# Kernel optimization log

Measured on AMD Instinct MI355X. Metric: run time of the kernel, lower is better.

## Reference

```python
import jax, jax.numpy as jnp
import numpy as np

D_MODEL = 1024
NUM_HEAD = 16
D_HEAD = 64
EPS = 1e-06


def setup_inputs() -> dict:
    key = jax.random.key(0)
    ks = jax.random.split(key, 16)
    d, h = D_MODEL, 4 * D_MODEL
    s = 1.0 / np.sqrt(d)
    inp = {
        "x": jax.random.normal(ks[0], (8, 1024, d), dtype=jnp.float32),
        # LayerNorm params
        "alpha1": jnp.ones((d,), jnp.float32),
        "beta1": jnp.zeros((d,), jnp.float32),
        "alpha2": jnp.ones((d,), jnp.float32),
        "beta2": jnp.zeros((d,), jnp.float32),
        # attention projections (weights stored as [in, out])
        "w_q": jax.random.normal(ks[1], (d, d), jnp.float32) * s,
        "b_q": jnp.zeros((d,), jnp.float32),
        "w_k": jax.random.normal(ks[2], (d, d), jnp.float32) * s,
        "b_k": jnp.zeros((d,), jnp.float32),
        "w_v": jax.random.normal(ks[3], (d, d), jnp.float32) * s,
        "b_v": jnp.zeros((d,), jnp.float32),
        "w_o": jax.random.normal(ks[4], (d, d), jnp.float32) * s,
        "b_o": jnp.zeros((d,), jnp.float32),
        # MLP
        "w1": jax.random.normal(ks[5], (d, h), jnp.float32) * s,
        "b1": jnp.zeros((h,), jnp.float32),
        "w2": jax.random.normal(ks[6], (h, d), jnp.float32) * (1.0 / np.sqrt(h)),
        "b2": jnp.zeros((d,), jnp.float32),
    }
    return inp


def _layer_norm(x, alpha, beta):
    mu = jnp.mean(x, axis=-1, keepdims=True)
    # torch .var() defaults to unbiased (ddof=1) — replicate exactly
    var = jnp.var(x, axis=-1, keepdims=True, ddof=1)
    return (x - mu) / jnp.sqrt(var + EPS) * alpha + beta


def _mha(x, w_q, b_q, w_k, b_k, w_v, b_v, w_o, b_o):
    b, p, _ = x.shape
    q = (x @ w_q + b_q).reshape(b, p, NUM_HEAD, D_HEAD).transpose(0, 2, 1, 3)
    k = (x @ w_k + b_k).reshape(b, p, NUM_HEAD, D_HEAD).transpose(0, 2, 1, 3)
    v = (x @ w_v + b_v).reshape(b, p, NUM_HEAD, D_HEAD).transpose(0, 2, 1, 3)
    scores = jnp.einsum("bhqd,bhkd->bhqk", q, k) / np.sqrt(D_HEAD).astype(np.float32)
    attn = jax.nn.softmax(scores, axis=-1)
    out = jnp.einsum("bhqk,bhkd->bhqd", attn, v)
    out = out.transpose(0, 2, 1, 3).reshape(b, p, NUM_HEAD * D_HEAD)
    return out @ w_o + b_o


def reference(x, alpha1, beta1, alpha2, beta2,
              w_q, b_q, w_k, b_k, w_v, b_v, w_o, b_o,
              w1, b1, w2, b2):
    # eval mode: Dropout is identity
    x = x + _mha(_layer_norm(x, alpha1, beta1), w_q, b_q, w_k, b_k, w_v, b_v, w_o, b_o)
    h = _layer_norm(x, alpha2, beta2)
    h = jax.nn.gelu(h @ w1 + b1, approximate=False)  # nn.GELU default: exact erf
    h = h @ w2 + b2
    return x + h
```

## Files before the change

kernel.cpp:

```cpp
#include <hip/hip_runtime.h>
#include <stdint.h>

typedef float f32x4 __attribute__((ext_vector_type(4)));
typedef short s16x8 __attribute__((ext_vector_type(8)));
typedef short s16x4 __attribute__((ext_vector_type(4)));
typedef unsigned int u32x4 __attribute__((ext_vector_type(4)));

#define M_TOTAL 8192
#define DM 1024
#define HID 4096
#define SEQ 1024
#define NH 16
#define DH 64

#define BAR() __builtin_amdgcn_s_barrier()
#define VMCNT8() do { asm volatile("s_waitcnt vmcnt(8)" ::: "memory"); __builtin_amdgcn_sched_barrier(0); } while (0)
#define VMCNT0() do { asm volatile("s_waitcnt vmcnt(0)" ::: "memory"); __builtin_amdgcn_sched_barrier(0); } while (0)
#define MFMA16 __builtin_amdgcn_mfma_f32_16x16x32_bf16

__device__ __forceinline__ unsigned short f2bf(float f) {
  unsigned int u = __float_as_uint(f);
  u = (u + 0x7fffu + ((u >> 16) & 1u)) >> 16;
  return (unsigned short)u;
}

__device__ __forceinline__ void gload16(const void* g, void* l) {
  __builtin_amdgcn_global_load_lds((__attribute__((address_space(1))) void*)g,
                                   (__attribute__((address_space(3))) void*)l,
                                   16, 0, 0);
}

__device__ __forceinline__ float erf_fast(float z) {
  const float az = fabsf(z);
  const float tt = 1.0f / fmaf(0.3275911f, az, 1.0f);
  float poly = fmaf(1.061405429f, tt, -1.453152027f);
  poly = fmaf(poly, tt, 1.421413741f);
  poly = fmaf(poly, tt, -0.284496736f);
  poly = fmaf(poly, tt, 0.254829592f);
  poly *= tt;
  const float e = __expf(-az * az);
  const float r = 1.0f - poly * e;
  return (z < 0.f) ? -r : r;
}

__global__ void tcast(const float* __restrict__ W, unsigned short* __restrict__ WT,
                      int K, int N) {
  __shared__ float tile[32][33];
  const int bn = blockIdx.x, bk = blockIdx.y;
  const int tx = threadIdx.x, ty = threadIdx.y;
#pragma unroll
  for (int i = 0; i < 32; i += 8)
    tile[ty + i][tx] = W[(size_t)(bk * 32 + ty + i) * N + bn * 32 + tx];
  __syncthreads();
#pragma unroll
  for (int i = 0; i < 32; i += 8)
    WT[(size_t)(bn * 32 + ty + i) * K + bk * 32 + tx] = f2bf(tile[tx][ty + i]);
}

__global__ __launch_bounds__(256)
void vtrans(const unsigned short* __restrict__ V, unsigned short* __restrict__ VT) {
  __shared__ unsigned short tile[64][65];
  const int bh = blockIdx.y, s0 = blockIdx.x * 64;
  const int t = threadIdx.x;
  const int sr = t >> 3, c0 = (t & 7) * 8;
#pragma unroll
  for (int it = 0; it < 2; ++it) {
    const int s = it * 32 + sr;
    const s16x8 v = *(const s16x8*)(V + ((size_t)bh * SEQ + s0 + s) * DH + c0);
#pragma unroll
    for (int i = 0; i < 8; ++i) tile[c0 + i][s] = (unsigned short)v[i];
  }
  __syncthreads();
#pragma unroll
  for (int it = 0; it < 2; ++it) {
    const int d = it * 32 + sr;
    s16x8 o;
#pragma unroll
    for (int i = 0; i < 8; ++i) o[i] = (short)tile[d][c0 + i];
    *(s16x8*)(VT + ((size_t)bh * DH + d) * SEQ + s0 + c0) = o;
  }
}

__global__ __launch_bounds__(256)
void ln_kernel(const float* __restrict__ x, const float* __restrict__ alpha,
               const float* __restrict__ beta, unsigned short* __restrict__ out) {
  const int row = blockIdx.x;
  const int t = threadIdx.x;
  const int w = t >> 6, lane = t & 63;
  const float4 v = ((const float4*)(x + (size_t)row * DM))[t];

  float s = v.x + v.y + v.z + v.w;
#pragma unroll
  for (int off = 32; off; off >>= 1) s += __shfl_xor(s, off, 64);
  __shared__ float red1[4];
  __shared__ float red2[4];
  if (lane == 0) red1[w] = s;
  __syncthreads();
  const float mu = (red1[0] + red1[1] + red1[2] + red1[3]) * (1.f / 1024.f);

  const float dx = v.x - mu, dy = v.y - mu, dz = v.z - mu, dw = v.w - mu;
  float sq = dx * dx + dy * dy + dz * dz + dw * dw;
#pragma unroll
  for (int off = 32; off; off >>= 1) sq += __shfl_xor(sq, off, 64);
  if (lane == 0) red2[w] = sq;
  __syncthreads();
  const float var = (red2[0] + red2[1] + red2[2] + red2[3]) * (1.f / 1023.f);
  const float rstd = rsqrtf(var + 1e-6f);

  const float4 a = ((const float4*)alpha)[t];
  const float4 b = ((const float4*)beta)[t];
  s16x4 o;
  o[0] = (short)f2bf(dx * rstd * a.x + b.x);
  o[1] = (short)f2bf(dy * rstd * a.y + b.y);
  o[2] = (short)f2bf(dz * rstd * a.z + b.z);
  o[3] = (short)f2bf(dw * rstd * a.w + b.w);
  *(s16x4*)(out + (size_t)row * DM + 4 * t) = o;
}

template <int MODE>
__device__ __forceinline__ void epi_store(int m, int n, float v, int Nout,
                                          unsigned short* __restrict__ obf, float* of,
                                          const float* res,
                                          const float* __restrict__ bias0,
                                          const float* __restrict__ bias1,
                                          const float* __restrict__ bias2) {
  if (MODE == 0) {
    const int which = n >> 10, nn = n & 1023;
    const float* bp = (which == 0) ? bias0 : ((which == 1) ? bias1 : bias2);
    v += bp[nn];
    const int b = m >> 10, s = m & 1023, h = nn >> 6, d = nn & 63;
    obf[(size_t)which * (M_TOTAL * DM) +
        (((size_t)(b * NH + h) * SEQ + s) * DH + d)] = f2bf(v);
  } else if (MODE == 1) {
    v += bias0[n] + res[(size_t)m * Nout + n];
    of[(size_t)m * Nout + n] = v;
  } else {
    v += bias0[n];
    const float gv = 0.5f * v * (1.0f + erf_fast(v * 0.70710678118654752f));
    obf[(size_t)m * Nout + n] = f2bf(gv);
  }
}

template <int MODE>
__global__ __launch_bounds__(256, 2)
void gemmk(const unsigned short* __restrict__ A, const unsigned short* __restrict__ B,
           int K, int Nout,
           unsigned short* __restrict__ obf, float* of, const float* res,
           const float* __restrict__ bias0, const float* __restrict__ bias1,
           const float* __restrict__ bias2) {
  __shared__ __attribute__((aligned(16))) unsigned short sA[2][128 * 64];
  __shared__ __attribute__((aligned(16))) unsigned short sB[2][128 * 64];
  const int t = threadIdx.x;
  const int lane = t & 63, wid = t >> 6;
  const int g = lane >> 4, r = lane & 15;
  const int wm = wid >> 1, wn = wid & 1;

  {
  }
  const int L = blockIdx.y * gridDim.x + blockIdx.x;
  const int nwg = gridDim.x * gridDim.y;
  const int chunk = nwg >> 3;
  const int ncols = chunk >> 6;
  const int denom = ncols << 3;
  const int xcd = L & 7, i = L >> 3;
  const int s = i / denom, w = i % denom;
  const int by = s * 8 + (w & 7);
  const int bx = xcd * ncols + (w >> 3);
  const int m0 = by * 128, n0 = bx * 128;

  const unsigned short* Ab = A + (size_t)m0 * K;
  const unsigned short* Bb = B + (size_t)n0 * K;

  const int rb = r & 7;
  const int slot0 = (g ^ rb) * 16;
  const int slot1 = ((4 + g) ^ rb) * 16;

  f32x4 acc[4][4];
#pragma unroll
  for (int i2 = 0; i2 < 4; ++i2)
#pragma unroll
    for (int j = 0; j < 4; ++j) acc[i2][j] = (f32x4){0.f, 0.f, 0.f, 0.f};

  auto stage = [&](int buf, int kt) {
#pragma unroll
    for (int s2 = 0; s2 < 4; ++s2) {
      const int f = s2 * 256 + t;
      const int row = f >> 3, c = f & 7;
      const int u = c ^ (row & 7);
      gload16(Ab + (size_t)row * K + kt * 64 + u * 8, &sA[buf][(size_t)row * 64 + c * 8]);
      gload16(Bb + (size_t)row * K + kt * 64 + u * 8, &sB[buf][(size_t)row * 64 + c * 8]);
    }
  };

  const int NT = K >> 6;
  stage(0, 0);
  stage(1, (NT > 1) ? 1 : 0);
  VMCNT8();
  BAR();

  for (int tt = 0; tt < NT; ++tt) {
    const int cur = tt & 1;
    const char* sAc = (const char*)&sA[cur][0];
    const char* sBc = (const char*)&sB[cur][0];

    s16x8 av[4][2], bv[4][2];
#pragma unroll
    for (int i2 = 0; i2 < 4; ++i2) {
      const int rbyte = (wm * 64 + i2 * 16 + r) * 128;
      av[i2][0] = *(const s16x8*)(sAc + rbyte + slot0);
      av[i2][1] = *(const s16x8*)(sAc + rbyte + slot1);
    }
#pragma unroll
    for (int n = 0; n < 4; ++n) {
      const int rbyte = (wn * 64 + n * 16 + r) * 128;
      bv[n][0] = *(const s16x8*)(sBc + rbyte + slot0);
      bv[n][1] = *(const s16x8*)(sBc + rbyte + slot1);
    }
#pragma unroll
    for (int i2 = 0; i2 < 4; ++i2)
#pragma unroll
      for (int n = 0; n < 4; ++n) {
        acc[i2][n] = MFMA16(av[i2][0], bv[n][0], acc[i2][n], 0, 0, 0);
        acc[i2][n] = MFMA16(av[i2][1], bv[n][1], acc[i2][n], 0, 0, 0);
      }

    BAR();
    const int tp2 = (tt + 2 < NT) ? tt + 2 : NT - 1;
    stage(cur, tp2);
    VMCNT8();
    BAR();
  }

  VMCNT0();

#pragma unroll
  for (int i2 = 0; i2 < 4; ++i2)
#pragma unroll
    for (int j = 0; j < 4; ++j) {
      const int m = m0 + wm * 64 + i2 * 16 + 4 * g + j;
#pragma unroll
      for (int nf = 0; nf < 4; ++nf) {
        const int n = n0 + wn * 64 + nf * 16 + r;
        epi_store<MODE>(m, n, acc[i2][nf][j], Nout, obf, of, res, bias0, bias1, bias2);
      }
    }
}

__global__ __launch_bounds__(256)
void attn_kernel(const unsigned short* __restrict__ QKV,
                 const unsigned short* __restrict__ VT,
                 unsigned short* __restrict__ O) {
  const unsigned short* Qg = QKV;
  const unsigned short* Kg = QKV + (size_t)M_TOTAL * DM;
  const int bh = blockIdx.y;
  const int q0 = blockIdx.x * 64;
  const int t = threadIdx.x, w = t >> 6, lane = t & 63;
  const int g = lane >> 4, r = lane & 15;
  const unsigned short* Qb = Qg + (size_t)bh * SEQ * DH;
  const unsigned short* Kb = Kg + (size_t)bh * SEQ * DH;
  const unsigned short* VTb = VT + (size_t)bh * DH * SEQ;

  __shared__ __attribute__((aligned(16))) unsigned short sK[2][64 * 64];
  __shared__ __attribute__((aligned(16))) unsigned short sV[2][64 * 64];

  s16x8 qf[2];
  {
    const unsigned short* qrow = Qb + (size_t)(q0 + w * 16 + r) * DH;
    qf[0] = *(const s16x8*)(qrow + g * 8);
    qf[1] = *(const s16x8*)(qrow + 32 + g * 8);
  }

  f32x4 oacc[4];
#pragma unroll
  for (int i = 0; i < 4; ++i) oacc[i] = (f32x4){0.f, 0.f, 0.f, 0.f};
  float mrun = -1e30f, lrun = 0.f;

  auto stage = [&](int buf, int kt) {
#pragma unroll
    for (int s2 = 0; s2 < 2; ++s2) {
      const int f = s2 * 256 + t;
      const int row = f >> 3, u = (f & 7) ^ (row & 7);
      gload16(Kb + (size_t)(kt * 64 + row) * DH + u * 8, &sK[buf][f * 8]);
      gload16(VTb + (size_t)row * SEQ + kt * 64 + u * 8, &sV[buf][f * 8]);
    }
  };

  stage(0, 0);
  __syncthreads();

  for (int kt = 0; kt < SEQ / 64; ++kt) {
    const int cur = kt & 1;
    if (kt < SEQ / 64 - 1) stage(cur ^ 1, kt + 1);

    f32x4 sc[4];
#pragma unroll
    for (int nf = 0; nf < 4; ++nf) {
      sc[nf] = (f32x4){0.f, 0.f, 0.f, 0.f};
      const int rowk = nf * 16 + r;
#pragma unroll
      for (int ks = 0; ks < 2; ++ks) {
        const int u = (4 * ks + g) ^ (rowk & 7);
        const s16x8 kf = *(const s16x8*)&sK[cur][rowk * 64 + u * 8];
        sc[nf] = __builtin_amdgcn_mfma_f32_16x16x32_bf16(kf, qf[ks], sc[nf], 0, 0, 0);
      }
    }

    float pm = -1e30f;
#pragma unroll
    for (int nf = 0; nf < 4; ++nf)
#pragma unroll
      for (int j = 0; j < 4; ++j) {
        sc[nf][j] *= 0.125f;
        pm = fmaxf(pm, sc[nf][j]);
      }
    pm = fmaxf(pm, __shfl_xor(pm, 16, 64));
    pm = fmaxf(pm, __shfl_xor(pm, 32, 64));

    const float mnew = fmaxf(mrun, pm);
    const float alpha = __expf(mrun - mnew);
    mrun = mnew;

    float p[4][4];
    float ps = 0.f;
#pragma unroll
    for (int nf = 0; nf < 4; ++nf)
#pragma unroll
      for (int j = 0; j < 4; ++j) {
        p[nf][j] = __expf(sc[nf][j] - mnew);
        ps += p[nf][j];
      }
    ps += __shfl_xor(ps, 16, 64);
    ps += __shfl_xor(ps, 32, 64);
    lrun = lrun * alpha + ps;

    float ao[4];
#pragma unroll
    for (int j = 0; j < 4; ++j) ao[j] = __shfl(alpha, 4 * g + j, 64);
#pragma unroll
    for (int nf2 = 0; nf2 < 4; ++nf2)
#pragma unroll
      for (int j = 0; j < 4; ++j) oacc[nf2][j] *= ao[j];

    unsigned int pk[4][2];
#pragma unroll
    for (int nf = 0; nf < 4; ++nf)
#pragma unroll
      for (int jp = 0; jp < 2; ++jp)
        pk[nf][jp] = (unsigned int)f2bf(p[nf][2 * jp]) |
                     ((unsigned int)f2bf(p[nf][2 * jp + 1]) << 16);

    unsigned int pa32[2][4];
#pragma unroll
    for (int ks = 0; ks < 2; ++ks)
#pragma unroll
      for (int q2 = 0; q2 < 4; ++q2) {
        const int src = r + 32 * (g & 1) + 16 * (q2 >> 1);
        const unsigned int a = (unsigned int)__shfl((int)pk[2 * ks][q2 & 1], src, 64);
        const unsigned int b = (unsigned int)__shfl((int)pk[2 * ks + 1][q2 & 1], src, 64);
        pa32[ks][q2] = (g >> 1) ? b : a;
      }
    s16x8 pa[2];
#pragma unroll
    for (int ks = 0; ks < 2; ++ks) {
      u32x4 pw;
      pw[0] = pa32[ks][0]; pw[1] = pa32[ks][1];
      pw[2] = pa32[ks][2]; pw[3] = pa32[ks][3];
      pa[ks] = __builtin_bit_cast(s16x8, pw);
    }

#pragma unroll
    for (int nf2 = 0; nf2 < 4; ++nf2) {
      const int rowd = nf2 * 16 + r;
#pragma unroll
      for (int ks = 0; ks < 2; ++ks) {
        const int u = (4 * ks + g) ^ (rowd & 7);
        const s16x8 vb = *(const s16x8*)&sV[cur][rowd * 64 + u * 8];
        oacc[nf2] = __builtin_amdgcn_mfma_f32_16x16x32_bf16(pa[ks], vb, oacc[nf2], 0, 0, 0);
      }
    }
    __syncthreads();
  }

  const int b = bh >> 4, h = bh & 15;
  const float linv = 1.f / lrun;
#pragma unroll
  for (int j = 0; j < 4; ++j) {
    const float lo = __shfl(linv, 4 * g + j, 64);
    const int q = q0 + w * 16 + 4 * g + j;
    const size_t orow = ((size_t)(b * SEQ + q)) * DM + h * DH;
#pragma unroll
    for (int nf2 = 0; nf2 < 4; ++nf2)
      O[orow + nf2 * 16 + r] = f2bf(oacc[nf2][j] * lo);
  }
}

extern "C" void kernel_launch(void* const* d_in, const int* in_sizes, int n_in,
                              void* d_out, int out_size, void* d_ws, size_t ws_size,
                              hipStream_t stream) {
  const float* x   = (const float*)d_in[0];
  const float* al1 = (const float*)d_in[1];
  const float* be1 = (const float*)d_in[2];
  const float* al2 = (const float*)d_in[3];
  const float* be2 = (const float*)d_in[4];
  const float* wq  = (const float*)d_in[5];
  const float* bq  = (const float*)d_in[6];
  const float* wk  = (const float*)d_in[7];
  const float* bk  = (const float*)d_in[8];
  const float* wv  = (const float*)d_in[9];
  const float* bv  = (const float*)d_in[10];
  const float* wo  = (const float*)d_in[11];
  const float* bo  = (const float*)d_in[12];
  const float* w1  = (const float*)d_in[13];
  const float* b1  = (const float*)d_in[14];
  const float* w2  = (const float*)d_in[15];
  const float* b2  = (const float*)d_in[16];
  float* dout = (float*)d_out;

  unsigned short* ws = (unsigned short*)d_ws;
  size_t off = 0;
  auto alloc = [&](size_t n) { unsigned short* p = ws + off; off += n; return p; };
  unsigned short* WTqkv = alloc((size_t)3072 * 1024);
  unsigned short* WTo   = alloc((size_t)1024 * 1024);
  unsigned short* WT1   = alloc((size_t)4096 * 1024);
  unsigned short* WT2   = alloc((size_t)1024 * 4096);
  unsigned short* xn    = alloc((size_t)M_TOTAL * DM);
  unsigned short* QKVb  = alloc((size_t)3 * M_TOTAL * DM);
  unsigned short* VTb   = alloc((size_t)M_TOTAL * DM);
  unsigned short* attn  = alloc((size_t)M_TOTAL * DM);
  unsigned short* h1    = alloc((size_t)M_TOTAL * HID);
  (void)ws_size; (void)in_sizes; (void)n_in; (void)out_size;

  const dim3 tb(32, 8);
  tcast<<<dim3(32, 32), tb, 0, stream>>>(wq, WTqkv, 1024, 1024);
  tcast<<<dim3(32, 32), tb, 0, stream>>>(wk, WTqkv + (size_t)1024 * 1024, 1024, 1024);
  tcast<<<dim3(32, 32), tb, 0, stream>>>(wv, WTqkv + (size_t)2048 * 1024, 1024, 1024);
  tcast<<<dim3(32, 32), tb, 0, stream>>>(wo, WTo, 1024, 1024);
  tcast<<<dim3(128, 32), tb, 0, stream>>>(w1, WT1, 1024, 4096);
  tcast<<<dim3(32, 128), tb, 0, stream>>>(w2, WT2, 4096, 1024);

  ln_kernel<<<M_TOTAL, 256, 0, stream>>>(x, al1, be1, xn);
  gemmk<0><<<dim3(24, 64), 256, 0, stream>>>(xn, WTqkv, 1024, 3072,
                                             QKVb, nullptr, nullptr, bq, bk, bv);
  vtrans<<<dim3(16, 128), 256, 0, stream>>>(QKVb + 2 * (size_t)M_TOTAL * DM, VTb);
  attn_kernel<<<dim3(16, 128), 256, 0, stream>>>(QKVb, VTb, attn);
  gemmk<1><<<dim3(8, 64), 256, 0, stream>>>(attn, WTo, 1024, 1024,
                                            nullptr, dout, x, bo, nullptr, nullptr);
  ln_kernel<<<M_TOTAL, 256, 0, stream>>>(dout, al2, be2, xn);
  gemmk<2><<<dim3(32, 64), 256, 0, stream>>>(xn, WT1, 1024, 4096,
                                             h1, nullptr, nullptr, b1, nullptr, nullptr);
  gemmk<1><<<dim3(8, 64), 256, 0, stream>>>(h1, WT2, 4096, 1024,
                                            nullptr, dout, dout, b2, nullptr, nullptr);
}
```

Baseline: 427.6 us.

## Load GEMM B operand directly from global into registers, stage only A in LDS

The GEMM kernel no longer stages the B tile through shared memory. Each wave loads its B fragments straight from global memory into registers, double-buffered across two register sets in a loop unrolled by two, while A keeps LDS double buffering. This halves LDS traffic and footprint, which could raise occupancy. In exchange, B is fetched redundantly by both wm waves and through uncoalesced per-lane 16-byte global loads, and the wait counts must track the new load mix.

New measurement: 623.2 us. 1.46x slower.

```diff
diff --git a/kernel.cpp b/kernel.cpp
--- a/kernel.cpp
+++ b/kernel.cpp
@@ -14,7 +14,8 @@
 #define DH 64
 
 #define BAR() __builtin_amdgcn_s_barrier()
-#define VMCNT8() do { asm volatile("s_waitcnt vmcnt(8)" ::: "memory"); __builtin_amdgcn_sched_barrier(0); } while (0)
+#define VMCNT4() do { asm volatile("s_waitcnt vmcnt(4)" ::: "memory"); __builtin_amdgcn_sched_barrier(0); } while (0)
+#define VMCNT12() do { asm volatile("s_waitcnt vmcnt(12)" ::: "memory"); __builtin_amdgcn_sched_barrier(0); } while (0)
 #define VMCNT0() do { asm volatile("s_waitcnt vmcnt(0)" ::: "memory"); __builtin_amdgcn_sched_barrier(0); } while (0)
 #define MFMA16 __builtin_amdgcn_mfma_f32_16x16x32_bf16
 
@@ -149,23 +150,20 @@
            const float* __restrict__ bias0, const float* __restrict__ bias1,
            const float* __restrict__ bias2) {
   __shared__ __attribute__((aligned(16))) unsigned short sA[2][128 * 64];
-  __shared__ __attribute__((aligned(16))) unsigned short sB[2][128 * 64];
   const int t = threadIdx.x;
   const int lane = t & 63, wid = t >> 6;
   const int g = lane >> 4, r = lane & 15;
   const int wm = wid >> 1, wn = wid & 1;
 
-  {
-  }
   const int L = blockIdx.y * gridDim.x + blockIdx.x;
   const int nwg = gridDim.x * gridDim.y;
   const int chunk = nwg >> 3;
   const int ncols = chunk >> 6;
   const int denom = ncols << 3;
-  const int xcd = L & 7, i = L >> 3;
-  const int s = i / denom, w = i % denom;
-  const int by = s * 8 + (w & 7);
-  const int bx = xcd * ncols + (w >> 3);
+  const int xcd = L & 7, li = L >> 3;
+  const int sst = li / denom, wst = li % denom;
+  const int by = sst * 8 + (wst & 7);
+  const int bx = xcd * ncols + (wst >> 3);
   const int m0 = by * 128, n0 = bx * 128;
 
   const unsigned short* Ab = A + (size_t)m0 * K;
@@ -175,35 +173,41 @@
   const int slot0 = (g ^ rb) * 16;
   const int slot1 = ((4 + g) ^ rb) * 16;
 
+  int boff[4][2];
+#pragma unroll
+  for (int nf = 0; nf < 4; ++nf)
+#pragma unroll
+    for (int ks = 0; ks < 2; ++ks)
+      boff[nf][ks] = (wn * 64 + nf * 16 + r) * K + ks * 32 + g * 8;
+
   f32x4 acc[4][4];
 #pragma unroll
   for (int i2 = 0; i2 < 4; ++i2)
 #pragma unroll
     for (int j = 0; j < 4; ++j) acc[i2][j] = (f32x4){0.f, 0.f, 0.f, 0.f};
 
-  auto stage = [&](int buf, int kt) {
+  auto stageA = [&](int buf, int kt) {
 #pragma unroll
     for (int s2 = 0; s2 < 4; ++s2) {
       const int f = s2 * 256 + t;
       const int row = f >> 3, c = f & 7;
       const int u = c ^ (row & 7);
       gload16(Ab + (size_t)row * K + kt * 64 + u * 8, &sA[buf][(size_t)row * 64 + c * 8]);
-      gload16(Bb + (size_t)row * K + kt * 64 + u * 8, &sB[buf][(size_t)row * 64 + c * 8]);
     }
   };
 
-  const int NT = K >> 6;
-  stage(0, 0);
-  stage(1, (NT > 1) ? 1 : 0);
-  VMCNT8();
-  BAR();
-
-  for (int tt = 0; tt < NT; ++tt) {
-    const int cur = tt & 1;
-    const char* sAc = (const char*)&sA[cur][0];
-    const char* sBc = (const char*)&sB[cur][0];
-
-    s16x8 av[4][2], bv[4][2];
+  s16x8 bA[4][2], bB[4][2];
+  auto loadB = [&](s16x8 (&bv)[4][2], int kt) {
+#pragma unroll
+    for (int nf = 0; nf < 4; ++nf)
+#pragma unroll
+      for (int ks = 0; ks < 2; ++ks)
+        bv[nf][ks] = *(const s16x8*)(Bb + (size_t)kt * 64 + boff[nf][ks]);
+  };
+
+  auto compute = [&](const unsigned short* sAbuf, const s16x8 (&bv)[4][2]) {
+    const char* sAc = (const char*)sAbuf;
+    s16x8 av[4][2];
 #pragma unroll
     for (int i2 = 0; i2 < 4; ++i2) {
       const int rbyte = (wm * 64 + i2 * 16 + r) * 128;
@@ -211,23 +215,42 @@
       av[i2][1] = *(const s16x8*)(sAc + rbyte + slot1);
     }
 #pragma unroll
-    for (int n = 0; n < 4; ++n) {
-      const int rbyte = (wn * 64 + n * 16 + r) * 128;
-      bv[n][0] = *(const s16x8*)(sBc + rbyte + slot0);
-      bv[n][1] = *(const s16x8*)(sBc + rbyte + slot1);
-    }
-#pragma unroll
     for (int i2 = 0; i2 < 4; ++i2)
 #pragma unroll
       for (int n = 0; n < 4; ++n) {
         acc[i2][n] = MFMA16(av[i2][0], bv[n][0], acc[i2][n], 0, 0, 0);
         acc[i2][n] = MFMA16(av[i2][1], bv[n][1], acc[i2][n], 0, 0, 0);
       }
-
+  };
+
+  const int NT = K >> 6;
+  stageA(0, 0);
+  loadB(bA, 0);
+  stageA(1, (NT > 1) ? 1 : 0);
+  VMCNT4();
+  BAR();
+
+  for (int tt = 0; tt < NT; tt += 2) {
+    compute(&sA[0][0], bA);
     BAR();
-    const int tp2 = (tt + 2 < NT) ? tt + 2 : NT - 1;
-    stage(cur, tp2);
-    VMCNT8();
+    {
+      const int tb = (tt + 1 < NT) ? tt + 1 : NT - 1;
+      const int ta = (tt + 2 < NT) ? tt + 2 : NT - 1;
+      loadB(bB, tb);
+      stageA(0, ta);
+    }
+    VMCNT12();
+    BAR();
+
+    compute(&sA[1][0], bB);
+    BAR();
+    {
+      const int tb = (tt + 2 < NT) ? tt + 2 : NT - 1;
+      const int ta = (tt + 3 < NT) ? tt + 3 : NT - 1;
+      loadB(bA, tb);
+      stageA(1, ta);
+    }
+    VMCNT12();
     BAR();
   }
 
```
